# Kernel optimization log

Measured on AMD Instinct MI355X. Metric: run time of the kernel, lower is better.

## Reference

```python
import jax, jax.numpy as jnp
import numpy as np

B, L, C = 64, 4096, 16
PL, PC, NP, D, FS = 128, 8, 64, 64, 100  # patch_size_L, patch_size_C, num_patches, output_dim, f_s


def setup_inputs() -> dict:
    key = jax.random.key(0)
    ks = jax.random.split(key, 9)
    x = jax.random.normal(ks[0], (B, L, C), dtype=jnp.float32)
    start_L = jax.random.randint(ks[1], (B, NP), 0, L - PL + 1, dtype=jnp.int32)
    idx_C = jax.random.randint(ks[2], (B, NP, PC), 0, C, dtype=jnp.int32)
    W1 = jax.random.normal(ks[3], (2 * PC + 1, D), dtype=jnp.float32) * 0.2
    b1 = jax.random.normal(ks[4], (D,), dtype=jnp.float32) * 0.02
    W2 = jax.random.normal(ks[5], (2 * D + 1, D), dtype=jnp.float32) * 0.1
    b2 = jax.random.normal(ks[6], (D,), dtype=jnp.float32) * 0.02
    W3 = jax.random.normal(ks[7], (PL * D, D), dtype=jnp.float32) * 0.01
    b3 = jax.random.normal(ks[8], (D,), dtype=jnp.float32) * 0.02
    return dict(x=x, start_L=start_L, idx_C=idx_C, W1=W1, b1=b1, W2=W2, b2=b2, W3=W3, b3=b3)


def reference(x, start_L, idx_C, W1, b1, W2, b2, W3, b3):
    T = 1.0 / FS
    # contiguous window indices along L (wrapped), [B, NP, PL]
    idx_L = (start_L[:, :, None] + jnp.arange(PL, dtype=jnp.int32)) % L
    # fused double gather: avoid materializing the [B, NP, L, C] broadcast of the original
    bidx = jnp.arange(B)[:, None, None, None]
    patches = x[bidx, idx_L[:, :, :, None], idx_C[:, :, None, :]]        # [B, NP, PL, PC]
    # time embedding: t = arange(L)*T gathered by idx_L
    t_patches = (idx_L.astype(jnp.float32) * T)[..., None]               # [B, NP, PL, 1]
    # channel embedding: c = arange(C) gathered by idx_C
    c_patches = jnp.broadcast_to(idx_C.astype(jnp.float32)[:, :, None, :], (B, NP, PL, PC))
    feats = jnp.concatenate([patches, t_patches, c_patches], axis=-1)    # [B, NP, PL, 2*PC+1]
    h = jax.nn.silu(feats @ W1 + b1)                                     # [B, NP, PL, D]
    # --- fft branch (computed then discarded by the original module; kept for fidelity) ---
    f = jnp.linspace(0.0, FS / 2.0, PL // 2 + 1)
    fft = jnp.fft.rfft(h, axis=-2, norm='ortho')                         # [B, NP, PL//2+1, D]
    f_patches = jnp.broadcast_to(f[None, None, :, None], (B, NP, PL // 2 + 1, 1))
    fcat = jnp.concatenate([fft.real, fft.imag, f_patches], axis=-1)     # [B, NP, PL//2+1, 2D+1]
    _unused = jax.nn.silu(fcat @ W2 + b2)
    # --- mixer on flattened patches ---
    flat = h.reshape(B, NP, PL * D)                                      # [B, NP, PL*D]
    out = jax.nn.silu(flat @ W3 + b3)                                    # [B, NP, D]
    return out
```

## Files before the change

### kernel.cpp

```cpp
#include <hip/hip_runtime.h>
#include <hip/hip_bf16.h>

#define BB 64
#define LL 4096
#define CC 16
#define PL 128
#define PC 8
#define NPP 64
#define DD 64
#define TSTEP 0.01f

#define PPB 32
#define KSPLIT 8
#define LT_PER (PL / KSPLIT)
#define NT_MAIN 256
#define NMB (BB * (NPP / PPB))

#define FRAG_U32 (PL * 8 * 256)
#define PART_FLT (KSPLIT * NMB * 2 * 64 * 16)
#define SPLIT_STRIDE (NMB * 2 * 64 * 16)

typedef float f32x4  __attribute__((ext_vector_type(4)));
typedef float f32x16 __attribute__((ext_vector_type(16)));
typedef int   i32x4  __attribute__((ext_vector_type(4)));
typedef unsigned int u32;

__device__ __forceinline__ float silu_f(float z) {
    return z * __builtin_amdgcn_rcpf(1.0f + __expf(-z));
}
__device__ __forceinline__ u32 pack_bf16(float lo, float hi) {
    __hip_bfloat162 p = __float22bfloat162_rn(float2{lo, hi});
    u32 r;
    __builtin_memcpy(&r, &p, 4);
    return r;
}

__global__ __launch_bounds__(256) void w3_prep(const float* __restrict__ W3,
                                               u32* __restrict__ wsf) {
    const int tid  = blockIdx.x * 256 + threadIdx.x;
    const int lane = tid & 63;
    const int m    = tid >> 6;
    const int ns   = m & 1;
    const int ksub = (m >> 1) & 1;
    const int kk   = (m >> 2) & 1;
    const int ltg  = m >> 3;
    const int k0   = ltg * 64 + kk * 32 + ksub * 16 + ((lane >> 5) << 3);
    const int col  = (ns << 5) + (lane & 31);
    u32 q[4];
    #pragma unroll
    for (int jj = 0; jj < 4; ++jj)
        q[jj] = pack_bf16(W3[(size_t)(k0 + 2 * jj)     * DD + col],
                          W3[(size_t)(k0 + 2 * jj + 1) * DD + col]);
    i32x4 v; v.x = (int)q[0]; v.y = (int)q[1]; v.z = (int)q[2]; v.w = (int)q[3];
    *(i32x4*)(wsf + (size_t)m * 256 + (lane << 2)) = v;
}

__global__ __launch_bounds__(NT_MAIN) void htfe_main(
    const float* __restrict__ x, const int* __restrict__ start_L,
    const int* __restrict__ idx_C, const float* __restrict__ W1,
    const float* __restrict__ b1, const u32* __restrict__ wsf,
    float* __restrict__ part)
{
    __shared__ __align__(16) u32   xq[LT_PER][PPB][4];
    __shared__ __align__(16) u32   hbuf[2][PPB][32];
    __shared__ __align__(16) float redbuf[2][64][16];
    __shared__ int sStart[PPB];
    __shared__ int sCi[PPB][PC];

    const int t    = threadIdx.x;
    const int lane = t & 63;
    const int w    = t >> 6;
    const int ns   = w & 1;
    const int kk   = w >> 1;

    const int mb    = blockIdx.x & (NMB - 1);
    const int split = blockIdx.x >> 7;
    const int b     = mb >> 1;
    const int p0    = (mb & 1) * PPB;
    const int lt0   = split * LT_PER;

    if (t < PPB) sStart[t] = start_L[b * NPP + p0 + t];
    if (t < PPB * PC) {
        const int pp = t >> 3, c = t & 7;
        sCi[pp][c] = idx_C[(size_t)((b * NPP + p0 + pp) << 3) + c];
    }
    __syncthreads();

    const int pA  = lane >> 2;
    const int pB2 = pA + 16;
    const int d0  = (w << 4) + ((lane & 3) << 2);
    float w1x[PC][4], w1t[4], cbA[4], cbB[4];
    {
        const f32x4 vt = *(const f32x4*)(W1 + PC * DD + d0);
        const f32x4 vb = *(const f32x4*)(b1 + d0);
        const float stA = (float)sStart[pA]  * TSTEP;
        const float stB = (float)sStart[pB2] * TSTEP;
        #pragma unroll
        for (int j = 0; j < 4; ++j) {
            w1t[j] = vt[j];
            cbA[j] = vb[j] + stA * vt[j];
            cbB[j] = vb[j] + stB * vt[j];
        }
        #pragma unroll
        for (int c = 0; c < PC; ++c) {
            const f32x4 vx = *(const f32x4*)(W1 + c * DD + d0);
            const f32x4 vc = *(const f32x4*)(W1 + (PC + 1 + c) * DD + d0);
            const float cfA = (float)sCi[pA][c];
            const float cfB = (float)sCi[pB2][c];
            #pragma unroll
            for (int j = 0; j < 4; ++j) {
                w1x[c][j] = vx[j];
                cbA[j] += cfA * vc[j];
                cbB[j] += cfB * vc[j];
            }
        }
    }

    #pragma unroll
    for (int uu = 0; uu < 2; ++uu) {
        const int u  = t * 2 + uu;
        const int lt = u >> 5;
        const int pp = u & 31;
        const float* xrow = x + ((size_t)b * LL + (size_t)(sStart[pp] + lt0 + lt)) * CC;
        u32 q[4];
        #pragma unroll
        for (int c2 = 0; c2 < 4; ++c2)
            q[c2] = pack_bf16(xrow[sCi[pp][2 * c2]], xrow[sCi[pp][2 * c2 + 1]]);
        i32x4 v; v.x = (int)q[0]; v.y = (int)q[1]; v.z = (int)q[2]; v.w = (int)q[3];
        *(i32x4*)&xq[lt][pp][0] = v;
    }
    __syncthreads();

    const int wrA = (pA << 7) + (((w << 5) + ((lane & 3) << 3)) ^ ((pA & 7) << 4));
    const int aRow = (lane & 31) << 7;
    const int aSwz = (lane & 7) << 4;
    const int cb0  = (kk << 6) + ((lane >> 5) << 4);
    const int aOff0 = aRow + (cb0 ^ aSwz);
    const int aOff1 = aRow + ((cb0 + 32) ^ aSwz);

    f32x16 acc = {};
    const u32* bsrc = wsf + ((size_t)lt0 * 8 + kk * 4 + ns) * 256 + (lane << 2);

    for (int lt = 0; lt < LT_PER; ++lt) {
        const int cur = lt & 1;

        const i32x4 bf0 = *(const i32x4*)(bsrc);
        const i32x4 bf1 = *(const i32x4*)(bsrc + 512);
        bsrc += 2048;

        const float tl = (float)(lt0 + lt) * TSTEP;
        const i32x4 qa = *(const i32x4*)&xq[lt][pA][0];
        const i32x4 qb = *(const i32x4*)&xq[lt][pB2][0];
        float aA[4], aB[4];
        #pragma unroll
        for (int j = 0; j < 4; ++j) {
            aA[j] = cbA[j] + tl * w1t[j];
            aB[j] = cbB[j] + tl * w1t[j];
        }
        #pragma unroll
        for (int c2 = 0; c2 < 4; ++c2) {
            const u32 ua = (u32)qa[c2], ub = (u32)qb[c2];
            const float xa0 = __uint_as_float(ua << 16);
            const float xa1 = __uint_as_float(ua & 0xffff0000u);
            const float xb0 = __uint_as_float(ub << 16);
            const float xb1 = __uint_as_float(ub & 0xffff0000u);
            #pragma unroll
            for (int j = 0; j < 4; ++j) {
                aA[j] += xa0 * w1x[2 * c2][j];
                aA[j] += xa1 * w1x[2 * c2 + 1][j];
                aB[j] += xb0 * w1x[2 * c2][j];
                aB[j] += xb1 * w1x[2 * c2 + 1][j];
            }
        }
        char* hb = (char*)&hbuf[cur][0][0];
        *(uint2*)(hb + wrA) =
            make_uint2(pack_bf16(silu_f(aA[0]), silu_f(aA[1])),
                       pack_bf16(silu_f(aA[2]), silu_f(aA[3])));
        *(uint2*)(hb + wrA + 2048) =
            make_uint2(pack_bf16(silu_f(aB[0]), silu_f(aB[1])),
                       pack_bf16(silu_f(aB[2]), silu_f(aB[3])));

        __syncthreads();

        const i32x4 af0 = *(const i32x4*)(hb + aOff0);
        const i32x4 af1 = *(const i32x4*)(hb + aOff1);
        asm("v_mfma_f32_32x32x16_bf16 %0, %1, %2, %0" : "+v"(acc) : "v"(af0), "v"(bf0));
        asm("v_mfma_f32_32x32x16_bf16 %0, %1, %2, %0" : "+v"(acc) : "v"(af1), "v"(bf1));
    }

    asm volatile("s_nop 7\ns_nop 7\ns_nop 7" ::);
    if (kk) {
        #pragma unroll
        for (int r4 = 0; r4 < 4; ++r4) {
            f32x4 v;
            v.x = acc[r4 * 4 + 0]; v.y = acc[r4 * 4 + 1];
            v.z = acc[r4 * 4 + 2]; v.w = acc[r4 * 4 + 3];
            *(f32x4*)&redbuf[ns][lane][r4 * 4] = v;
        }
    }
    __syncthreads();
    if (!kk) {
        float* pdst = part + ((((size_t)split * NMB + mb) * 2 + ns) * 64 + lane) * 16;
        #pragma unroll
        for (int r4 = 0; r4 < 4; ++r4) {
            const f32x4 v = *(const f32x4*)&redbuf[ns][lane][r4 * 4];
            f32x4 o;
            o.x = acc[r4 * 4 + 0] + v.x; o.y = acc[r4 * 4 + 1] + v.y;
            o.z = acc[r4 * 4 + 2] + v.z; o.w = acc[r4 * 4 + 3] + v.w;
            *(f32x4*)(pdst + r4 * 4) = o;
        }
    }
}

__global__ __launch_bounds__(256) void finish_reduce(const float* __restrict__ part,
                                                     const float* __restrict__ b3,
                                                     float* __restrict__ out) {
    const int tid  = blockIdx.x * 256 + threadIdx.x;
    const int rq   = tid & 3;
    const int lane = (tid >> 2) & 63;
    const int ns   = (tid >> 8) & 1;
    const int mb   = tid >> 9;
    const float* src = part + (((size_t)mb * 2 + ns) * 64 + lane) * 16 + rq * 4;
    f32x4 s = {0.f, 0.f, 0.f, 0.f};
    #pragma unroll
    for (int split = 0; split < KSPLIT; ++split) {
        const f32x4 v = *(const f32x4*)(src + (size_t)split * SPLIT_STRIDE);
        s.x += v.x; s.y += v.y; s.z += v.z; s.w += v.w;
    }
    const int col  = (ns << 5) + (lane & 31);
    const float bias = b3[col];
    #pragma unroll
    for (int j = 0; j < 4; ++j) {
        const int prow = j + 8 * rq + 4 * (lane >> 5);
        out[(size_t)(mb * 32 + prow) * DD + col] = silu_f(s[j] + bias);
    }
}

extern "C" void kernel_launch(void* const* d_in, const int* in_sizes, int n_in,
                              void* d_out, int out_size, void* d_ws, size_t ws_size,
                              hipStream_t stream) {
    const float* x       = (const float*)d_in[0];
    const int*   start_L = (const int*)  d_in[1];
    const int*   idx_C   = (const int*)  d_in[2];
    const float* W1      = (const float*)d_in[3];
    const float* b1      = (const float*)d_in[4];
    const float* W3      = (const float*)d_in[7];
    const float* b3      = (const float*)d_in[8];
    float* out  = (float*)d_out;
    u32*   wsf  = (u32*)d_ws;
    float* part = (float*)(wsf + FRAG_U32);

    w3_prep<<<256, 256, 0, stream>>>(W3, wsf);
    htfe_main<<<NMB * KSPLIT, NT_MAIN, 0, stream>>>(x, start_L, idx_C, W1, b1, wsf, part);
    finish_reduce<<<256, 256, 0, stream>>>(part, b3, out);
}
```

Before: 40.23 us.

## Compute first-layer features with MFMA and pass h via permlane swaps

The first linear layer (x, time and channel features times W1) now runs on MFMA instructions in bf16, using a hi/lo split of x and time for accuracy. The SiLU output is repacked into A-fragments in registers with permlane32 swaps instead of going through shared memory with a barrier per step. Each block now covers all 64 patches of a batch with KSPLIT raised to 16, so the grid and partial-sum layout change. This removes per-iteration syncthreads and the scalar FMA work, but the first layer now carries bf16 rounding error and twice the partial sums must be reduced.

```diff
diff --git a/kernel.cpp b/kernel.cpp
--- a/kernel.cpp
+++ b/kernel.cpp
@@ -10,29 +10,44 @@
 #define DD 64
 #define TSTEP 0.01f
 
-#define PPB 32
-#define KSPLIT 8
+#define KSPLIT 16
 #define LT_PER (PL / KSPLIT)
 #define NT_MAIN 256
-#define NMB (BB * (NPP / PPB))
+#define NMB BB
 
 #define FRAG_U32 (PL * 8 * 256)
-#define PART_FLT (KSPLIT * NMB * 2 * 64 * 16)
-#define SPLIT_STRIDE (NMB * 2 * 64 * 16)
+#define SPLIT_STRIDE (NMB * 2 * 2 * 64 * 16)
+#define PART_FLT (KSPLIT * SPLIT_STRIDE)
 
 typedef float f32x4  __attribute__((ext_vector_type(4)));
 typedef float f32x16 __attribute__((ext_vector_type(16)));
 typedef int   i32x4  __attribute__((ext_vector_type(4)));
+typedef short s16x8  __attribute__((ext_vector_type(8)));
 typedef unsigned int u32;
 
+__device__ __forceinline__ u32 f2bf(float f) {
+    u32 u = __float_as_uint(f);
+    return (u + 0x7fffu + ((u >> 16) & 1u)) >> 16;
+}
 __device__ __forceinline__ float silu_f(float z) {
     return z * __builtin_amdgcn_rcpf(1.0f + __expf(-z));
 }
-__device__ __forceinline__ u32 pack_bf16(float lo, float hi) {
+__device__ __forceinline__ u32 pk(float lo, float hi) {
     __hip_bfloat162 p = __float22bfloat162_rn(float2{lo, hi});
     u32 r;
     __builtin_memcpy(&r, &p, 4);
     return r;
+}
+__device__ __forceinline__ s16x8 as8(i32x4 v) {
+    s16x8 r;
+    __builtin_memcpy(&r, &v, 16);
+    return r;
+}
+__device__ __forceinline__ void plswap(u32& a, u32& b) {
+    auto r = __builtin_amdgcn_permlane32_swap(a, b, false, false);
+    u32 tmp[2];
+    __builtin_memcpy(tmp, &r, 8);
+    a = tmp[0]; b = tmp[1];
 }
 
 __global__ __launch_bounds__(256) void w3_prep(const float* __restrict__ W3,
@@ -49,8 +64,8 @@
     u32 q[4];
     #pragma unroll
     for (int jj = 0; jj < 4; ++jj)
-        q[jj] = pack_bf16(W3[(size_t)(k0 + 2 * jj)     * DD + col],
-                          W3[(size_t)(k0 + 2 * jj + 1) * DD + col]);
+        q[jj] = pk(W3[(size_t)(k0 + 2 * jj)     * DD + col],
+                   W3[(size_t)(k0 + 2 * jj + 1) * DD + col]);
     i32x4 v; v.x = (int)q[0]; v.y = (int)q[1]; v.z = (int)q[2]; v.w = (int)q[3];
     *(i32x4*)(wsf + (size_t)m * 256 + (lane << 2)) = v;
 }
@@ -61,153 +76,149 @@
     const float* __restrict__ b1, const u32* __restrict__ wsf,
     float* __restrict__ part)
 {
-    __shared__ __align__(16) u32   xq[LT_PER][PPB][4];
-    __shared__ __align__(16) u32   hbuf[2][PPB][32];
-    __shared__ __align__(16) float redbuf[2][64][16];
-    __shared__ int sStart[PPB];
-    __shared__ int sCi[PPB][PC];
+    __shared__ __align__(16) u32    xqf[LT_PER * 64 * 8];
+    __shared__ __align__(16) f32x16 redacc[2][2][64];
+    __shared__ int sStart[64];
+    __shared__ int sCi[64][PC];
 
     const int t    = threadIdx.x;
     const int lane = t & 63;
     const int w    = t >> 6;
-    const int ns   = w & 1;
     const int kk   = w >> 1;
+    const int ph   = w & 1;
+    const int l31  = lane & 31;
+    const bool loH = lane < 32;
 
     const int mb    = blockIdx.x & (NMB - 1);
-    const int split = blockIdx.x >> 7;
-    const int b     = mb >> 1;
-    const int p0    = (mb & 1) * PPB;
+    const int split = blockIdx.x >> 6;
+    const int b     = mb;
     const int lt0   = split * LT_PER;
 
-    if (t < PPB) sStart[t] = start_L[b * NPP + p0 + t];
-    if (t < PPB * PC) {
-        const int pp = t >> 3, c = t & 7;
-        sCi[pp][c] = idx_C[(size_t)((b * NPP + p0 + pp) << 3) + c];
+    if (t < 64) sStart[t] = start_L[b * NPP + t];
+    {
+        const int i0 = t, i1 = t + 256;
+        sCi[i0 >> 3][i0 & 7] = idx_C[(size_t)b * NPP * PC + i0];
+        sCi[i1 >> 3][i1 & 7] = idx_C[(size_t)b * NPP * PC + i1];
     }
     __syncthreads();
 
-    const int pA  = lane >> 2;
-    const int pB2 = pA + 16;
-    const int d0  = (w << 4) + ((lane & 3) << 2);
-    float w1x[PC][4], w1t[4], cbA[4], cbB[4];
-    {
-        const f32x4 vt = *(const f32x4*)(W1 + PC * DD + d0);
-        const f32x4 vb = *(const f32x4*)(b1 + d0);
-        const float stA = (float)sStart[pA]  * TSTEP;
-        const float stB = (float)sStart[pB2] * TSTEP;
+    const int p  = ph * 32 + l31;
+    const int dA = kk * 32 + l31;
+    const float startPf = (float)sStart[p];
+
+    i32x4 a1f0, a1f1;
+    if (loH) {
+        a1f0.x = (int)pk(W1[0 * DD + dA], W1[1 * DD + dA]);
+        a1f0.y = (int)pk(W1[2 * DD + dA], W1[3 * DD + dA]);
+        a1f0.z = (int)pk(W1[4 * DD + dA], W1[5 * DD + dA]);
+        a1f0.w = (int)pk(W1[6 * DD + dA], W1[7 * DD + dA]);
+        a1f1.x = (int)pk(W1[8 * DD + dA], W1[8 * DD + dA]);
+        a1f1.y = (int)pk(b1[dA], 0.0f);
+        a1f1.z = 0; a1f1.w = 0;
+    } else {
+        a1f0.x = (int)pk(W1[ 9 * DD + dA], W1[10 * DD + dA]);
+        a1f0.y = (int)pk(W1[11 * DD + dA], W1[12 * DD + dA]);
+        a1f0.z = (int)pk(W1[13 * DD + dA], W1[14 * DD + dA]);
+        a1f0.w = (int)pk(W1[15 * DD + dA], W1[16 * DD + dA]);
+        a1f1.x = (int)pk(W1[0 * DD + dA], W1[1 * DD + dA]);
+        a1f1.y = (int)pk(W1[2 * DD + dA], W1[3 * DD + dA]);
+        a1f1.z = (int)pk(W1[4 * DD + dA], W1[5 * DD + dA]);
+        a1f1.w = (int)pk(W1[6 * DD + dA], W1[7 * DD + dA]);
+    }
+    i32x4 cReg;
+    cReg.x = (int)pk((float)sCi[p][0], (float)sCi[p][1]);
+    cReg.y = (int)pk((float)sCi[p][2], (float)sCi[p][3]);
+    cReg.z = (int)pk((float)sCi[p][4], (float)sCi[p][5]);
+    cReg.w = (int)pk((float)sCi[p][6], (float)sCi[p][7]);
+
+    #pragma unroll
+    for (int uu = 0; uu < 2; ++uu) {
+        const int u  = t * 2 + uu;
+        const int lt = u >> 6;
+        const int pp = u & 63;
+        const float* xrow = x + ((size_t)b * LL + (size_t)(sStart[pp] + lt0 + lt)) * CC;
+        u32 qh[4], ql[4];
         #pragma unroll
-        for (int j = 0; j < 4; ++j) {
-            w1t[j] = vt[j];
-            cbA[j] = vb[j] + stA * vt[j];
-            cbB[j] = vb[j] + stB * vt[j];
+        for (int c2 = 0; c2 < 4; ++c2) {
+            const float v0 = xrow[sCi[pp][2 * c2]];
+            const float v1 = xrow[sCi[pp][2 * c2 + 1]];
+            const u32 h0 = f2bf(v0), h1 = f2bf(v1);
+            qh[c2] = h0 | (h1 << 16);
+            ql[c2] = f2bf(v0 - __uint_as_float(h0 << 16)) |
+                     (f2bf(v1 - __uint_as_float(h1 << 16)) << 16);
         }
+        const int swz = ((pp >> 2) & 1) << 2;
+        u32* dst = xqf + lt * 512 + pp * 8;
+        i32x4 vh; vh.x=(int)qh[0]; vh.y=(int)qh[1]; vh.z=(int)qh[2]; vh.w=(int)qh[3];
+        i32x4 vl; vl.x=(int)ql[0]; vl.y=(int)ql[1]; vl.z=(int)ql[2]; vl.w=(int)ql[3];
+        *(i32x4*)(dst + (0 ^ swz)) = vh;
+        *(i32x4*)(dst + (4 ^ swz)) = vl;
+    }
+    __syncthreads();
+
+    f32x16 acc0 = {}, acc1 = {};
+    const u32* bsrc = wsf + ((size_t)lt0 * 8 + (size_t)kk * 4) * 256 + (lane << 2);
+    const u32 ONEP = pk(1.0f, 0.0f);
+    const u32* xrd = xqf + p * 8 + ((((lane >> 5) << 2) ^ (((p >> 2) & 1) << 2)));
+
+    #pragma unroll 2
+    for (int lt = 0; lt < LT_PER; ++lt) {
+        const i32x4 bf00 = *(const i32x4*)(bsrc);
+        const i32x4 bf01 = *(const i32x4*)(bsrc + 256);
+        const i32x4 bf10 = *(const i32x4*)(bsrc + 512);
+        const i32x4 bf11 = *(const i32x4*)(bsrc + 768);
+        bsrc += 2048;
+
+        const i32x4 rd = *(const i32x4*)(xrd + lt * 512);
+
+        const float tf  = (startPf + (float)(lt0 + lt)) * TSTEP;
+        const u32   tb  = f2bf(tf);
+        const u32   tpk2 = tb | (f2bf(tf - __uint_as_float(tb << 16)) << 16);
+        i32x4 tvec; tvec.x = (int)tpk2; tvec.y = (int)ONEP; tvec.z = 0; tvec.w = 0;
+
+        const i32x4 b0f = loH ? rd : cReg;
+        const i32x4 b1f = loH ? tvec : rd;
+
+        f32x16 hp = {};
+        hp = __builtin_amdgcn_mfma_f32_32x32x16_bf16(as8(a1f0), as8(b0f), hp, 0, 0, 0);
+        hp = __builtin_amdgcn_mfma_f32_32x32x16_bf16(as8(a1f1), as8(b1f), hp, 0, 0, 0);
+
+        u32 P[8];
         #pragma unroll
-        for (int c = 0; c < PC; ++c) {
-            const f32x4 vx = *(const f32x4*)(W1 + c * DD + d0);
-            const f32x4 vc = *(const f32x4*)(W1 + (PC + 1 + c) * DD + d0);
-            const float cfA = (float)sCi[pA][c];
-            const float cfB = (float)sCi[pB2][c];
+        for (int j = 0; j < 8; ++j)
+            P[j] = pk(silu_f(hp[2 * j]), silu_f(hp[2 * j + 1]));
+
+        plswap(P[0], P[2]); plswap(P[1], P[3]);
+        plswap(P[4], P[6]); plswap(P[5], P[7]);
+        i32x4 af0; af0.x=(int)P[0]; af0.y=(int)P[1]; af0.z=(int)P[2]; af0.w=(int)P[3];
+        i32x4 af1; af1.x=(int)P[4]; af1.y=(int)P[5]; af1.z=(int)P[6]; af1.w=(int)P[7];
+
+        acc0 = __builtin_amdgcn_mfma_f32_32x32x16_bf16(as8(af0), as8(bf00), acc0, 0, 0, 0);
+        acc0 = __builtin_amdgcn_mfma_f32_32x32x16_bf16(as8(af1), as8(bf10), acc0, 0, 0, 0);
+        acc1 = __builtin_amdgcn_mfma_f32_32x32x16_bf16(as8(af0), as8(bf01), acc1, 0, 0, 0);
+        acc1 = __builtin_amdgcn_mfma_f32_32x32x16_bf16(as8(af1), as8(bf11), acc1, 0, 0, 0);
+    }
+
+    if (kk == 1) {
+        redacc[ph][0][lane] = acc0;
+        redacc[ph][1][lane] = acc1;
+    }
+    __syncthreads();
+    if (kk == 0) {
+        const f32x16 r0 = redacc[ph][0][lane];
+        const f32x16 r1 = redacc[ph][1][lane];
+        float* pd0 = part + ((((size_t)split * NMB + mb) * 2 + ph) * 2 + 0) * 1024 + (lane << 4);
+        float* pd1 = pd0 + 1024;
+        #pragma unroll
+        for (int q = 0; q < 4; ++q) {
+            f32x4 o0, o1;
             #pragma unroll
             for (int j = 0; j < 4; ++j) {
-                w1x[c][j] = vx[j];
-                cbA[j] += cfA * vc[j];
-                cbB[j] += cfB * vc[j];
+                o0[j] = acc0[q * 4 + j] + r0[q * 4 + j];
+                o1[j] = acc1[q * 4 + j] + r1[q * 4 + j];
             }
-        }
-    }
-
-    #pragma unroll
-    for (int uu = 0; uu < 2; ++uu) {
-        const int u  = t * 2 + uu;
-        const int lt = u >> 5;
-        const int pp = u & 31;
-        const float* xrow = x + ((size_t)b * LL + (size_t)(sStart[pp] + lt0 + lt)) * CC;
-        u32 q[4];
-        #pragma unroll
-        for (int c2 = 0; c2 < 4; ++c2)
-            q[c2] = pack_bf16(xrow[sCi[pp][2 * c2]], xrow[sCi[pp][2 * c2 + 1]]);
-        i32x4 v; v.x = (int)q[0]; v.y = (int)q[1]; v.z = (int)q[2]; v.w = (int)q[3];
-        *(i32x4*)&xq[lt][pp][0] = v;
-    }
-    __syncthreads();
-
-    const int wrA = (pA << 7) + (((w << 5) + ((lane & 3) << 3)) ^ ((pA & 7) << 4));
-    const int aRow = (lane & 31) << 7;
-    const int aSwz = (lane & 7) << 4;
-    const int cb0  = (kk << 6) + ((lane >> 5) << 4);
-    const int aOff0 = aRow + (cb0 ^ aSwz);
-    const int aOff1 = aRow + ((cb0 + 32) ^ aSwz);
-
-    f32x16 acc = {};
-    const u32* bsrc = wsf + ((size_t)lt0 * 8 + kk * 4 + ns) * 256 + (lane << 2);
-
-    for (int lt = 0; lt < LT_PER; ++lt) {
-        const int cur = lt & 1;
-
-        const i32x4 bf0 = *(const i32x4*)(bsrc);
-        const i32x4 bf1 = *(const i32x4*)(bsrc + 512);
-        bsrc += 2048;
-
-        const float tl = (float)(lt0 + lt) * TSTEP;
-        const i32x4 qa = *(const i32x4*)&xq[lt][pA][0];
-        const i32x4 qb = *(const i32x4*)&xq[lt][pB2][0];
-        float aA[4], aB[4];
-        #pragma unroll
-        for (int j = 0; j < 4; ++j) {
-            aA[j] = cbA[j] + tl * w1t[j];
-            aB[j] = cbB[j] + tl * w1t[j];
-        }
-        #pragma unroll
-        for (int c2 = 0; c2 < 4; ++c2) {
-            const u32 ua = (u32)qa[c2], ub = (u32)qb[c2];
-            const float xa0 = __uint_as_float(ua << 16);
-            const float xa1 = __uint_as_float(ua & 0xffff0000u);
-            const float xb0 = __uint_as_float(ub << 16);
-            const float xb1 = __uint_as_float(ub & 0xffff0000u);
-            #pragma unroll
-            for (int j = 0; j < 4; ++j) {
-                aA[j] += xa0 * w1x[2 * c2][j];
-                aA[j] += xa1 * w1x[2 * c2 + 1][j];
-                aB[j] += xb0 * w1x[2 * c2][j];
-                aB[j] += xb1 * w1x[2 * c2 + 1][j];
-            }
-        }
-        char* hb = (char*)&hbuf[cur][0][0];
-        *(uint2*)(hb + wrA) =
-            make_uint2(pack_bf16(silu_f(aA[0]), silu_f(aA[1])),
-                       pack_bf16(silu_f(aA[2]), silu_f(aA[3])));
-        *(uint2*)(hb + wrA + 2048) =
-            make_uint2(pack_bf16(silu_f(aB[0]), silu_f(aB[1])),
-                       pack_bf16(silu_f(aB[2]), silu_f(aB[3])));
-
-        __syncthreads();
-
-        const i32x4 af0 = *(const i32x4*)(hb + aOff0);
-        const i32x4 af1 = *(const i32x4*)(hb + aOff1);
-        asm("v_mfma_f32_32x32x16_bf16 %0, %1, %2, %0" : "+v"(acc) : "v"(af0), "v"(bf0));
-        asm("v_mfma_f32_32x32x16_bf16 %0, %1, %2, %0" : "+v"(acc) : "v"(af1), "v"(bf1));
-    }
-
-    asm volatile("s_nop 7\ns_nop 7\ns_nop 7" ::);
-    if (kk) {
-        #pragma unroll
-        for (int r4 = 0; r4 < 4; ++r4) {
-            f32x4 v;
-            v.x = acc[r4 * 4 + 0]; v.y = acc[r4 * 4 + 1];
-            v.z = acc[r4 * 4 + 2]; v.w = acc[r4 * 4 + 3];
-            *(f32x4*)&redbuf[ns][lane][r4 * 4] = v;
-        }
-    }
-    __syncthreads();
-    if (!kk) {
-        float* pdst = part + ((((size_t)split * NMB + mb) * 2 + ns) * 64 + lane) * 16;
-        #pragma unroll
-        for (int r4 = 0; r4 < 4; ++r4) {
-            const f32x4 v = *(const f32x4*)&redbuf[ns][lane][r4 * 4];
-            f32x4 o;
-            o.x = acc[r4 * 4 + 0] + v.x; o.y = acc[r4 * 4 + 1] + v.y;
-            o.z = acc[r4 * 4 + 2] + v.z; o.w = acc[r4 * 4 + 3] + v.w;
-            *(f32x4*)(pdst + r4 * 4) = o;
+            *(f32x4*)(pd0 + q * 4) = o0;
+            *(f32x4*)(pd1 + q * 4) = o1;
         }
     }
 }
@@ -219,20 +230,22 @@
     const int rq   = tid & 3;
     const int lane = (tid >> 2) & 63;
     const int ns   = (tid >> 8) & 1;
-    const int mb   = tid >> 9;
-    const float* src = part + (((size_t)mb * 2 + ns) * 64 + lane) * 16 + rq * 4;
+    const int ph   = (tid >> 9) & 1;
+    const int mb   = tid >> 10;
+    const int l31  = lane & 31;
+    const float* src = part + (((size_t)mb * 2 + ph) * 2 + ns) * 1024 + (lane << 4) + (rq << 2);
     f32x4 s = {0.f, 0.f, 0.f, 0.f};
     #pragma unroll
-    for (int split = 0; split < KSPLIT; ++split) {
-        const f32x4 v = *(const f32x4*)(src + (size_t)split * SPLIT_STRIDE);
+    for (int sp = 0; sp < KSPLIT; ++sp) {
+        const f32x4 v = *(const f32x4*)(src + (size_t)sp * SPLIT_STRIDE);
         s.x += v.x; s.y += v.y; s.z += v.z; s.w += v.w;
     }
-    const int col  = (ns << 5) + (lane & 31);
+    const int col  = (ns << 5) + l31;
     const float bias = b3[col];
     #pragma unroll
     for (int j = 0; j < 4; ++j) {
-        const int prow = j + 8 * rq + 4 * (lane >> 5);
-        out[(size_t)(mb * 32 + prow) * DD + col] = silu_f(s[j] + bias);
+        const int prow = ph * 32 + j + 8 * rq + 4 * (lane >> 5);
+        out[((size_t)mb * NPP + prow) * DD + col] = silu_f(s[j] + bias);
     }
 }
 
```

After: 38.30 us. -4.8%, faster.
